# Kernel tuning notes

Measured on AMD Instinct MI355X. Metric: run time of the kernel, lower is better.

## Reference

```python
import jax, jax.numpy as jnp
import numpy as np

B, L, F, H, NC = 128, 1024, 128, 64, 16


def setup_inputs() -> dict:
    key = jax.random.key(0)
    ks = jax.random.split(key, 8)
    # strictly increasing timestamps -> each unique_consecutive group holds exactly
    # one event, so the torch group-mean over agg_c_t is a plain per-event update.
    t = jnp.broadcast_to(jnp.arange(L, dtype=jnp.float32), (B, L))
    m = jax.random.randint(ks[0], (B, L), 0, F).astype(jnp.float32)  # feature ids stored as float
    x = jax.random.normal(ks[1], (B, L), dtype=jnp.float32)
    delt = jax.random.uniform(ks[2], (B, L), dtype=jnp.float32)
    X = jnp.stack([t, m, x, delt], axis=1)  # [B, 4, L]
    lengths = jnp.full((B,), L, dtype=jnp.int32)
    s = 1.0 / np.sqrt(H + 1)
    W_gates = jax.random.uniform(ks[3], (F, 4 * H, H + 1), minval=-s, maxval=s)  # per-feature Linear(H+1 -> 4H)
    b_gates = jax.random.uniform(ks[4], (F, 4 * H), minval=-s, maxval=s)
    w_decay = jax.random.uniform(ks[5], (F,), minval=-1.0, maxval=1.0)  # per-feature Linear(1 -> 1)
    b_decay = jax.random.uniform(ks[6], (F,), minval=-1.0, maxval=1.0)
    in_dim = F * H + H  # concat(c_t, h_t.flatten()) -- default output branch
    so = 1.0 / np.sqrt(in_dim)
    W_out = jax.random.uniform(ks[7], (NC, in_dim), minval=-so, maxval=so)
    b_out = jnp.zeros((NC,), dtype=jnp.float32)
    return dict(X=X, lengths=lengths, W_gates=W_gates, b_gates=b_gates,
                w_decay=w_decay, b_decay=b_decay, W_out=W_out, b_out=b_out)


def _run_sample(x, delt, m, length, W_gates, b_gates, w_decay, b_decay):
    """Event-wise recurrence for one sample; returns concat(c_t, h_t.flatten())."""
    L_ = x.shape[0]
    F_, _, Hp1 = W_gates.shape
    H_ = Hp1 - 1

    def step(carry, ev):
        h_t, c_t = carry                     # h_t: [F,H], c_t: [H]
        mj, xj, dj, valid = ev
        # gated per-feature decay: exp(-max(0, w*dt + b)) (sr == 1)
        decay = jnp.exp(-jnp.maximum(0.0, w_decay[mj] * dj + b_decay[mj]))
        h_dec = decay * h_t[mj]
        inp = jnp.concatenate([xj[None], h_dec])            # [H+1]
        gates = W_gates[mj] @ inp + b_gates[mj]             # [4H]
        gi, gf, go, gc = jnp.split(gates, 4)
        c_new = jax.nn.sigmoid(gf) * c_t + jax.nn.sigmoid(gi) * jnp.tanh(gc)
        h_row = jax.nn.sigmoid(go) * jnp.tanh(c_new)
        c_t = jnp.where(valid, c_new, c_t)
        h_t = h_t.at[mj].set(jnp.where(valid, h_row, h_t[mj]))
        return (h_t, c_t), None

    valid = jnp.arange(L_) < length
    init = (jnp.zeros((F_, H_), x.dtype), jnp.zeros((H_,), x.dtype))
    (h_t, c_t), _ = jax.lax.scan(step, init, (m, x, delt, valid))
    return jnp.concatenate([c_t, h_t.reshape(-1)])          # [F*H + H]


def reference(X, lengths, W_gates, b_gates, w_decay, b_decay, W_out, b_out):
    m = X[:, 1].astype(jnp.int32)
    x = X[:, 2]
    delt = X[:, 3]
    feat = jax.vmap(lambda xi, di, mi, li: _run_sample(
        xi, di, mi, li, W_gates, b_gates, w_decay, b_decay))(x, delt, m, lengths)
    logits = feat @ W_out.T + b_out                          # [B, n_class]
    return jax.nn.softmax(logits, axis=-1)                   # torch softmax(dim=0) on 1-D vec per sample
```

## Files before the change

kernel.cpp:

```cpp
#include <hip/hip_runtime.h>
#include <cstdint>
#include <cstddef>

#define Bn 128
#define Ln 1024
#define Fn 128
#define Hn 64
#define NGn 256
#define NCn 16
#define IN_DIM (Hn + Fn*Hn)
#define NT 512
#define NREF 7
#define RING 64

typedef float    f32x4 __attribute__((ext_vector_type(4)));
typedef float    f32x2 __attribute__((ext_vector_type(2)));
typedef _Float16 f16x8 __attribute__((ext_vector_type(8)));
typedef _Float16 f16x2 __attribute__((ext_vector_type(2)));

union U8 { f16x8 v; f16x2 p[4]; };

#define OFF_AB   0
#define OFF_GO   65536
#define OFF_H    98304
#define OFF_PK   114688
#define OFF_CN   122880
#define OFF_MF   139264
#define OFF_PV   140288
#define OFF_NX   142336
#define OFF_RDY  144384
#define OFF_DON  145408
#define OFF_C    146432
#define OFF_RED  146688
#define OFF_LOG  147200
#define LDS_TOTAL 147264

__device__ __forceinline__ float fsigm(float x) {
    return __fdividef(1.0f, 1.0f + __expf(-x));
}
__device__ __forceinline__ float ftanh(float x) {
    float e = __expf(2.0f * x);
    return 1.0f - __fdividef(2.0f, e + 1.0f);
}
__device__ __forceinline__ float sigm_slow(float x) { return 1.0f / (1.0f + expf(-x)); }

#if __has_builtin(__builtin_amdgcn_fdot2)
#define DOT2(WP, HP, ACC) __builtin_amdgcn_fdot2((WP), (HP), (ACC), false)
#else
#define DOT2(WP, HP, ACC) fmaf((float)(WP)[0], (float)(HP)[0], \
                               fmaf((float)(WP)[1], (float)(HP)[1], (ACC)))
#endif

__global__ __launch_bounds__(256)
void prep_f16(const float* __restrict__ Wg, const float* __restrict__ bg,
              f16x8* __restrict__ Gw, f32x2* __restrict__ Gwb)
{
    const int m = blockIdx.x, r = threadIdx.x;
    const float* src = Wg + ((size_t)m * NGn + r) * 65;
    f32x2 wb; wb[0] = src[0]; wb[1] = bg[m * NGn + r];
    Gwb[((size_t)m << 8) + r] = wb;
#pragma unroll
    for (int c = 0; c < 8; ++c) {
        f16x8 v;
#pragma unroll
        for (int e = 0; e < 8; ++e) v[e] = (_Float16)src[1 + 8 * c + e];
        Gw[((size_t)m << 11) + (c << 8) + r] = v;
    }
}

__global__ __launch_bounds__(NT, 1)
void lstm_pre(const float* __restrict__ X, const int* __restrict__ lengths,
              const f16x8* __restrict__ Gw, const f32x2* __restrict__ Gwb,
              const float* __restrict__ wdec, const float* __restrict__ bdec,
              const float* __restrict__ Wo, const float* __restrict__ bo,
              float* __restrict__ out)
{
    extern __shared__ char smem[];
    float*    AB_s = (float*)(smem + OFF_AB);
    float*    GO_s = (float*)(smem + OFF_GO);
    _Float16* h16  = (_Float16*)(smem + OFF_H);
    f32x2*    pk_s = (f32x2*)(smem + OFF_PK);
    float*    CN_s = (float*)(smem + OFF_CN);
    unsigned char* mf_s = (unsigned char*)(smem + OFF_MF);
    short*         pv_s = (short*)(smem + OFF_PV);
    short*         nx_s = (short*)(smem + OFF_NX);
    unsigned char* rdy  = (unsigned char*)(smem + OFF_RDY);
    unsigned char* don  = (unsigned char*)(smem + OFF_DON);
    float* c_s = (float*)(smem + OFF_C);
    int*   fo_s = (int*)(smem + OFF_RED);
    float* red_lds   = (float*)(smem + OFF_RED);
    float* logit_lds = (float*)(smem + OFF_LOG);

    const int b   = blockIdx.x;
    const int tid = threadIdx.x;
    const int l   = tid & 63;
    const int w   = tid >> 6;

    const float* mrow = X + ((size_t)b * 4 + 1) * Ln;
    const float* xrow = X + ((size_t)b * 4 + 2) * Ln;
    const float* drow = X + ((size_t)b * 4 + 3) * Ln;

    int len = lengths[b];
    if (len > Ln) len = Ln;

    if (tid < Fn) { AB_s[tid] = wdec[tid]; AB_s[Fn + tid] = bdec[tid]; }
    if (tid < Fn) fo_s[tid] = Ln;
    __syncthreads();
    for (int jj = tid; jj < Ln; jj += NT) {
        const int   m   = (int)mrow[jj];
        const float dec = __expf(-fmaxf(0.0f, fmaf(AB_s[m], drow[jj], AB_s[Fn + m])));
        f32x2 t; t[0] = xrow[jj]; t[1] = dec;
        pk_s[jj] = t;
        mf_s[jj] = (unsigned char)m;
        nx_s[jj] = -1;
        rdy[jj] = 0; don[jj] = 0;
    }
    __syncthreads();
    for (int j0 = tid; j0 < Ln; j0 += NT) {
        const int mm = (int)mf_s[j0];
        short pv = -1;
        for (int k = j0 - 1; k >= 0; --k)
            if ((int)mf_s[k] == mm) { pv = (short)k; break; }
        pv_s[j0] = pv;
        if (j0 < len) atomicMin(&fo_s[mm], j0);
    }
    __syncthreads();
    for (int j0 = tid; j0 < Ln; j0 += NT) {
        const int p = (int)pv_s[j0];
        if (p >= 0) nx_s[p] = (short)j0;
    }
    {
        f16x8 hzv;
#pragma unroll
        for (int e = 0; e < 8; ++e) hzv[e] = (_Float16)0.0f;
        for (int i = tid; i < (Fn * Hn / 8); i += NT) ((f16x8*)h16)[i] = hzv;
    }
    __syncthreads();
    for (int e = tid; e < Fn * Hn; e += NT) {
        const int m = e >> 6, u = e & 63;
        const int f0 = fo_s[m];
        if (f0 < len) {
            const float xv = pk_s[f0][0];
            const f32x2* bp = Gwb + ((size_t)m << 8) + u;
            const f32x2 wi = bp[0], wf = bp[64], wo = bp[128], wc = bp[192];
            const float gi = fmaf(xv, wi[0], wi[1]);
            const float gf = fmaf(xv, wf[0], wf[1]);
            const float go = fmaf(xv, wo[0], wo[1]);
            const float gc = fmaf(xv, wc[0], wc[1]);
            AB_s[(m << 7) + (u << 1)]     = fsigm(gf);
            AB_s[(m << 7) + (u << 1) + 1] = fsigm(gi) * ftanh(gc);
            GO_s[(m << 6) + u]            = fsigm(go);
        }
    }
    __syncthreads();

    if (w == 0) {
        __builtin_amdgcn_s_setprio(1);
        float cu = 0.0f;
        if (len > 0) {
            const int i1 = (1 < len) ? 1 : len - 1;
            const int i2 = (2 < len) ? 2 : len - 1;
            int m0 = (int)mf_s[0],  m1 = (int)mf_s[i1], m2 = (int)mf_s[i2];
            int pv0 = (int)pv_s[0], pv1 = (int)pv_s[i1], pv2 = (int)pv_s[i2];
            int df0 = 1;
            int df1 = (pv1 < 0) ? 1 : (int)*(volatile unsigned char*)(don + ((pv1 < 0) ? 0 : pv1));
            int df2 = (pv2 < 0) ? 1 : (int)*(volatile unsigned char*)(don + ((pv2 < 0) ? 0 : pv2));
            asm volatile("" ::: "memory");
            f32x2 ab0 = *(const f32x2*)(AB_s + (m0 << 7) + (l << 1));
            f32x2 ab1 = *(const f32x2*)(AB_s + (m1 << 7) + (l << 1));
            f32x2 ab2 = *(const f32x2*)(AB_s + (m2 << 7) + (l << 1));
            for (int j = 0; j < len; ++j) {
                const int j3 = (j + 3 < len) ? j + 3 : len - 1;
                const int m3 = (int)mf_s[j3];
                const int pv3 = (int)pv_s[j3];
                const int pvc = (pv3 < 0) ? 0 : pv3;
                const int dq  = (int)*(volatile unsigned char*)(don + pvc);
                const int df3 = (pv3 < 0) ? 1 : dq;
                if (j3 >= RING) {
                    if (*(volatile unsigned char*)(don + (j3 - RING)) == 0) {
                        while (*(volatile unsigned char*)(don + (j3 - RING)) == 0)
                            asm volatile("s_sleep 1");
                    }
                }
                asm volatile("" ::: "memory");
                f32x2 ab3 = *(const f32x2*)(AB_s + (m3 << 7) + (l << 1));
                if (!df0) {
                    while (*(volatile unsigned char*)(don + pv0) == 0)
                        asm volatile("s_sleep 1");
                    asm volatile("" ::: "memory");
                    ab0 = *(const f32x2*)(AB_s + (m0 << 7) + (l << 1));
                }
                const float cn = fmaf(ab0[0], cu, ab0[1]);
                cu = cn;
                CN_s[((j & (RING - 1)) << 6) + l] = cn;
                asm volatile("" ::: "memory");
                if (l == 0) *(volatile unsigned char*)(rdy + j) = 1;
                m0 = m1; pv0 = pv1; df0 = df1; ab0 = ab1;
                m1 = m2; pv1 = pv2; df1 = df2; ab1 = ab2;
                m2 = m3; pv2 = pv3; df2 = df3; ab2 = ab3;
            }
        }
        __builtin_amdgcn_s_setprio(0);
        c_s[l] = cu;
    } else {
        for (int q = w - 1; q < len; q += NREF) {
            const int m  = (int)mf_s[q];
            const int jn = (int)nx_s[q];
            f16x8 wreg[32];
            float xv = 0.0f, dc = 0.0f;
            f32x2 wbi, wbf, wbo, wbc;
            if (jn >= 0) {
#pragma unroll
                for (int g = 0; g < 4; ++g) {
                    const f16x8* wp = Gw + ((size_t)m << 11) + (g << 6) + l;
#pragma unroll
                    for (int c = 0; c < 8; ++c) wreg[g * 8 + c] = wp[c << 8];
                }
                const f32x2 pkn = pk_s[jn];
                xv = pkn[0]; dc = pkn[1];
                const f32x2* bp = Gwb + ((size_t)m << 8) + l;
                wbi = bp[0]; wbf = bp[64]; wbo = bp[128]; wbc = bp[192];
            }
            while (*(volatile unsigned char*)(rdy + q) == 0)
                asm volatile("s_sleep 1");
            asm volatile("" ::: "memory");
            const float cnq = CN_s[((q & (RING - 1)) << 6) + l];
            const float gov = GO_s[(m << 6) + l];
            const float hv  = gov * ftanh(cnq);
            h16[(m << 6) + l] = (_Float16)hv;
            asm volatile("" ::: "memory");
            if (jn >= 0) {
                U8 hr[8];
                {
                    const f16x8* hp = (const f16x8*)(h16 + (m << 6));
#pragma unroll
                    for (int c = 0; c < 8; ++c) hr[c].v = hp[c];
                }
                float a0 = 0.f, a1 = 0.f, a2 = 0.f, a3 = 0.f;
#pragma unroll
                for (int c = 0; c < 8; ++c) {
                    U8 w0, w1, w2, w3;
                    w0.v = wreg[c]; w1.v = wreg[8 + c];
                    w2.v = wreg[16 + c]; w3.v = wreg[24 + c];
#pragma unroll
                    for (int e = 0; e < 4; ++e) {
                        a0 = DOT2(w0.p[e], hr[c].p[e], a0);
                        a1 = DOT2(w1.p[e], hr[c].p[e], a1);
                        a2 = DOT2(w2.p[e], hr[c].p[e], a2);
                        a3 = DOT2(w3.p[e], hr[c].p[e], a3);
                    }
                }
                const float gi = fmaf(dc, a0, fmaf(xv, wbi[0], wbi[1]));
                const float gf = fmaf(dc, a1, fmaf(xv, wbf[0], wbf[1]));
                const float go = fmaf(dc, a2, fmaf(xv, wbo[0], wbo[1]));
                const float gc = fmaf(dc, a3, fmaf(xv, wbc[0], wbc[1]));
                AB_s[(m << 7) + (l << 1)]     = fsigm(gf);
                AB_s[(m << 7) + (l << 1) + 1] = fsigm(gi) * ftanh(gc);
                GO_s[(m << 6) + l]            = fsigm(go);
            }
            asm volatile("" ::: "memory");
            if (l == 0) *(volatile unsigned char*)(don + q) = 1;
        }
    }
    __syncthreads();

    float p[NCn];
#pragma unroll
    for (int c = 0; c < NCn; ++c) p[c] = 0.0f;
    for (int i = tid; i < IN_DIM; i += NT) {
        const float fv = (i < Hn) ? c_s[i] : (float)h16[i - Hn];
#pragma unroll
        for (int c = 0; c < NCn; ++c)
            p[c] = fmaf(Wo[(size_t)c * IN_DIM + i], fv, p[c]);
    }
#pragma unroll
    for (int c = 0; c < NCn; ++c) {
        float v = p[c];
#pragma unroll
        for (int off = 32; off > 0; off >>= 1) v += __shfl_down(v, off, 64);
        if (l == 0) red_lds[w * NCn + c] = v;
    }
    __syncthreads();
    if (tid < NCn) {
        float s = bo[tid];
#pragma unroll
        for (int sw = 0; sw < (NT / 64); ++sw) s += red_lds[sw * NCn + tid];
        logit_lds[tid] = s;
    }
    __syncthreads();
    if (tid == 0) {
        float mx = logit_lds[0];
        for (int c = 1; c < NCn; ++c) mx = fmaxf(mx, logit_lds[c]);
        float e[NCn], sm = 0.0f;
        for (int c = 0; c < NCn; ++c) { e[c] = expf(logit_lds[c] - mx); sm += e[c]; }
        const float inv = 1.0f / sm;
        for (int c = 0; c < NCn; ++c) out[(size_t)b * NCn + c] = e[c] * inv;
    }
}

__global__ __launch_bounds__(256)
void lstm_fallback(const float* __restrict__ X, const int* __restrict__ lengths,
                   const float* __restrict__ Wg, const float* __restrict__ bg,
                   const float* __restrict__ wdec, const float* __restrict__ bdec,
                   const float* __restrict__ Wo, const float* __restrict__ bo,
                   float* __restrict__ out)
{
    __shared__ __align__(16) float h_lds[Fn * Hn];
    __shared__ float c_lds[Hn];
    __shared__ int   m_lds[Ln];
    __shared__ float x_lds[Ln];
    __shared__ float d_lds[Ln];
    __shared__ float wd_lds[Fn], bd_lds[Fn];
    __shared__ float red_lds[4 * NCn];
    __shared__ float logit_lds[NCn];

    const int b   = blockIdx.x;
    const int tid = threadIdx.x;
    const int l   = tid & 63;
    const int w   = tid >> 6;
    const int q   = l & 3;
    const int u   = w * 16 + (l >> 2);

    const float* mrow = X + ((size_t)b * 4 + 1) * Ln;
    const float* xrow = X + ((size_t)b * 4 + 2) * Ln;
    const float* drow = X + ((size_t)b * 4 + 3) * Ln;

    for (int i = tid; i < Fn * Hn; i += 256) h_lds[i] = 0.0f;
    if (tid < Hn) c_lds[tid] = 0.0f;
    if (tid < Fn) { wd_lds[tid] = wdec[tid]; bd_lds[tid] = bdec[tid]; }
    for (int i = tid; i < Ln; i += 256) {
        m_lds[i] = (int)mrow[i];
        x_lds[i] = xrow[i];
        d_lds[i] = drow[i];
    }
    __syncthreads();

    int len = lengths[b];
    if (len > Ln) len = Ln;
    const int g_raw = q * 64 + u;

    for (int j = 0; j < len; ++j) {
        const int   mj = m_lds[j];
        const float xj = x_lds[j];
        const float dj = d_lds[j];
        const float dec = expf(-fmaxf(0.0f, fmaf(wd_lds[mj], dj, bd_lds[mj])));
        const float4* hp = (const float4*)(h_lds + mj * Hn);
        const float* row = Wg + ((size_t)mj * NGn + g_raw) * 65;
        float acc = fmaf(row[0], xj, bg[mj * NGn + g_raw]);
        float a0 = 0.f, a1 = 0.f, a2 = 0.f, a3 = 0.f;
#pragma unroll
        for (int k4 = 0; k4 < 16; ++k4) {
            float4 hv = hp[k4];
            a0 = fmaf(row[1 + 4*k4 + 0], hv.x, a0);
            a1 = fmaf(row[1 + 4*k4 + 1], hv.y, a1);
            a2 = fmaf(row[1 + 4*k4 + 2], hv.z, a2);
            a3 = fmaf(row[1 + 4*k4 + 3], hv.w, a3);
        }
        acc = fmaf(dec, (a0 + a1) + (a2 + a3), acc);
        const int base = l & ~3;
        const float gi = __shfl(acc, base + 0, 64);
        const float gf = __shfl(acc, base + 1, 64);
        const float go = __shfl(acc, base + 2, 64);
        const float gc = __shfl(acc, base + 3, 64);
        __syncthreads();
        const float c_new = fmaf(sigm_slow(gf), c_lds[u], sigm_slow(gi) * tanhf(gc));
        if (q == 0) {
            c_lds[u] = c_new;
            h_lds[mj * Hn + u] = sigm_slow(go) * tanhf(c_new);
        }
        __syncthreads();
    }

    float p[NCn];
#pragma unroll
    for (int c = 0; c < NCn; ++c) p[c] = 0.0f;
    for (int i = tid; i < IN_DIM; i += 256) {
        const float fv = (i < Hn) ? c_lds[i] : h_lds[i - Hn];
#pragma unroll
        for (int c = 0; c < NCn; ++c)
            p[c] = fmaf(Wo[(size_t)c * IN_DIM + i], fv, p[c]);
    }
#pragma unroll
    for (int c = 0; c < NCn; ++c) {
        float v = p[c];
#pragma unroll
        for (int off = 32; off > 0; off >>= 1) v += __shfl_down(v, off, 64);
        if (l == 0) red_lds[w * NCn + c] = v;
    }
    __syncthreads();
    if (tid < NCn) {
        logit_lds[tid] = red_lds[tid] + red_lds[NCn + tid] +
                         red_lds[2 * NCn + tid] + red_lds[3 * NCn + tid] + bo[tid];
    }
    __syncthreads();
    if (tid == 0) {
        float mx = logit_lds[0];
        for (int c = 1; c < NCn; ++c) mx = fmaxf(mx, logit_lds[c]);
        float e[NCn], s = 0.0f;
        for (int c = 0; c < NCn; ++c) { e[c] = expf(logit_lds[c] - mx); s += e[c]; }
        const float inv = 1.0f / s;
        for (int c = 0; c < NCn; ++c) out[(size_t)b * NCn + c] = e[c] * inv;
    }
}

extern "C" void kernel_launch(void* const* d_in, const int* in_sizes, int n_in,
                              void* d_out, int out_size, void* d_ws, size_t ws_size,
                              hipStream_t stream)
{
    const float* X      = (const float*)d_in[0];
    const int*   len    = (const int*)  d_in[1];
    const float* Wg     = (const float*)d_in[2];
    const float* bg     = (const float*)d_in[3];
    const float* wdec   = (const float*)d_in[4];
    const float* bdec   = (const float*)d_in[5];
    const float* Wo     = (const float*)d_in[6];
    const float* bo     = (const float*)d_in[7];
    float*       out    = (float*)d_out;

    const size_t gw_bytes  = (size_t)Fn * 2048 * sizeof(f16x8);
    const size_t gwb_bytes = (size_t)Fn * 256 * sizeof(f32x2);
    const size_t need      = gw_bytes + gwb_bytes;

    if (ws_size >= need) {
        f16x8* Gw  = (f16x8*)d_ws;
        f32x2* Gwb = (f32x2*)((char*)d_ws + gw_bytes);
        prep_f16<<<Fn, 256, 0, stream>>>(Wg, bg, Gw, Gwb);
        (void)hipFuncSetAttribute((const void*)lstm_pre,
                                  hipFuncAttributeMaxDynamicSharedMemorySize,
                                  LDS_TOTAL);
        lstm_pre<<<Bn, NT, LDS_TOTAL, stream>>>(X, len, Gw, Gwb,
                                                wdec, bdec, Wo, bo, out);
    } else {
        lstm_fallback<<<Bn, 256, 0, stream>>>(X, len, Wg, bg,
                                              wdec, bdec, Wo, bo, out);
    }
}
```

Measured before the change: 490.5 us.

## Double refiner waves and prefetch next event's gate weights after signaling

Raises the block size from 512 to 1024 threads, so the number of refiner wavefronts working on events round-robin goes from 7 to 15, and enlarges the reduction scratch area to match. The refiner loop now loads the next event's per-feature gate weights, biases and inputs right after publishing the done flag for the current event. Previously these loads were issued at the top of each iteration. The aim is more events in flight and weight-load latency hidden behind the wait for the serial cell chain. The cost is higher register pressure: each wave carries 128 registers of f16 weights, which at 1024 threads per block could force spills or lower occupancy.

```diff
diff --git a/kernel.cpp b/kernel.cpp
--- a/kernel.cpp
+++ b/kernel.cpp
@@ -9,8 +9,8 @@
 #define NGn 256
 #define NCn 16
 #define IN_DIM (Hn + Fn*Hn)
-#define NT 512
-#define NREF 7
+#define NT 1024
+#define NREF 15
 #define RING 64
 
 typedef float    f32x4 __attribute__((ext_vector_type(4)));
@@ -32,8 +32,8 @@
 #define OFF_DON  145408
 #define OFF_C    146432
 #define OFF_RED  146688
-#define OFF_LOG  147200
-#define LDS_TOTAL 147264
+#define OFF_LOG  147712
+#define LDS_TOTAL 147776
 
 __device__ __forceinline__ float fsigm(float x) {
     return __fdividef(1.0f, 1.0f + __expf(-x));
@@ -203,24 +203,29 @@
         __builtin_amdgcn_s_setprio(0);
         c_s[l] = cu;
     } else {
-        for (int q = w - 1; q < len; q += NREF) {
-            const int m  = (int)mf_s[q];
-            const int jn = (int)nx_s[q];
-            f16x8 wreg[32];
-            float xv = 0.0f, dc = 0.0f;
-            f32x2 wbi, wbf, wbo, wbc;
-            if (jn >= 0) {
+        int q = w - 1;
+        f16x8 wreg[32];
+        float xv = 0.0f, dc = 0.0f;
+        f32x2 wbi, wbf, wbo, wbc;
+        int jn_cur = -1;
+        if (q < len) {
+            const int m = (int)mf_s[q];
+            jn_cur = (int)nx_s[q];
+            if (jn_cur >= 0) {
 #pragma unroll
                 for (int g = 0; g < 4; ++g) {
                     const f16x8* wp = Gw + ((size_t)m << 11) + (g << 6) + l;
 #pragma unroll
                     for (int c = 0; c < 8; ++c) wreg[g * 8 + c] = wp[c << 8];
                 }
-                const f32x2 pkn = pk_s[jn];
+                const f32x2 pkn = pk_s[jn_cur];
                 xv = pkn[0]; dc = pkn[1];
                 const f32x2* bp = Gwb + ((size_t)m << 8) + l;
                 wbi = bp[0]; wbf = bp[64]; wbo = bp[128]; wbc = bp[192];
             }
+        }
+        while (q < len) {
+            const int m = (int)mf_s[q];
             while (*(volatile unsigned char*)(rdy + q) == 0)
                 asm volatile("s_sleep 1");
             asm volatile("" ::: "memory");
@@ -229,7 +234,7 @@
             const float hv  = gov * ftanh(cnq);
             h16[(m << 6) + l] = (_Float16)hv;
             asm volatile("" ::: "memory");
-            if (jn >= 0) {
+            if (jn_cur >= 0) {
                 U8 hr[8];
                 {
                     const f16x8* hp = (const f16x8*)(h16 + (m << 6));
@@ -260,6 +265,24 @@
             }
             asm volatile("" ::: "memory");
             if (l == 0) *(volatile unsigned char*)(don + q) = 1;
+            const int q2 = q + NREF;
+            if (q2 < len) {
+                const int m2 = (int)mf_s[q2];
+                jn_cur = (int)nx_s[q2];
+                if (jn_cur >= 0) {
+#pragma unroll
+                    for (int g = 0; g < 4; ++g) {
+                        const f16x8* wp = Gw + ((size_t)m2 << 11) + (g << 6) + l;
+#pragma unroll
+                        for (int c = 0; c < 8; ++c) wreg[g * 8 + c] = wp[c << 8];
+                    }
+                    const f32x2 pkn = pk_s[jn_cur];
+                    xv = pkn[0]; dc = pkn[1];
+                    const f32x2* bp = Gwb + ((size_t)m2 << 8) + l;
+                    wbi = bp[0]; wbf = bp[64]; wbo = bp[128]; wbc = bp[192];
+                }
+            }
+            q = q2;
         }
     }
     __syncthreads();
```

After: 998.7 us. +103.6%, slower.
